# Optimization experiments

Hardware: AMD Instinct MI355X
Metric: run time of the kernel (lower is better)

## Reference

```python
import jax, jax.numpy as jnp
import numpy as np

N = 20000      # nodes
E = 640000     # edges (before self loops)
IN = 256       # in_channels == out_channels (forced by classifier size 4*in)
H1, C1 = 8, 16   # conv1: heads=8, out=16 -> concat 128
H2, C2 = 1, 256  # conv2: heads=1, out=out_channels
B = 4096       # article pairs
NEG_SLOPE = 0.2  # PyG GATv2Conv default negative_slope


def setup_inputs() -> dict:
    key = jax.random.key(0)
    ks = jax.random.split(key, 24)
    s = 0.05
    inp = {
        "gnn_x": jax.random.normal(ks[0], (N, IN), jnp.float32),
        "vanilla_x": jax.random.normal(ks[1], (N, IN), jnp.float32),
        "edge_src": jax.random.randint(ks[2], (E,), 0, N, jnp.int32),
        "edge_dst": jax.random.randint(ks[3], (E,), 0, N, jnp.int32),
        "a1_idx": jax.random.randint(ks[4], (B,), 0, N, jnp.int64),
        "a2_idx": jax.random.randint(ks[5], (B,), 0, N, jnp.int64),
        # conv1 params (lin_l, lin_r, att, bias)
        "Wl1": jax.random.normal(ks[6], (IN, H1 * C1), jnp.float32) * s,
        "bl1": jnp.zeros((H1 * C1,), jnp.float32),
        "Wr1": jax.random.normal(ks[7], (IN, H1 * C1), jnp.float32) * s,
        "br1": jnp.zeros((H1 * C1,), jnp.float32),
        "att1": jax.random.normal(ks[8], (H1, C1), jnp.float32) * s,
        "bias1": jnp.zeros((H1 * C1,), jnp.float32),
        # conv2 params
        "Wl2": jax.random.normal(ks[9], (H1 * C1, H2 * C2), jnp.float32) * s,
        "bl2": jnp.zeros((H2 * C2,), jnp.float32),
        "Wr2": jax.random.normal(ks[10], (H1 * C1, H2 * C2), jnp.float32) * s,
        "br2": jnp.zeros((H2 * C2,), jnp.float32),
        "att2": jax.random.normal(ks[11], (H2, C2), jnp.float32) * s,
        "bias2": jnp.zeros((H2 * C2,), jnp.float32),
        # classifier
        "Wc": jax.random.normal(ks[12], (4 * IN, 1), jnp.float32) * s,
        "bc": jnp.zeros((1,), jnp.float32),
    }
    return inp


def _gatv2_layer(x, src, dst, Wl, bl, Wr, br, att, bias):
    """GATv2Conv: x_l = lin_l(x)[src], x_r = lin_r(x)[dst];
    e = att . leaky_relu(x_l + x_r); segment softmax over dst; scatter-add x_l*alpha."""
    n = x.shape[0]
    h, c = att.shape
    xl = (x @ Wl + bl).reshape(n, h, c)
    xr = (x @ Wr + br).reshape(n, h, c)
    # per-edge attention logits [E, H]
    e = jnp.einsum('ehc,hc->eh', jax.nn.leaky_relu(xl[src] + xr[dst], NEG_SLOPE), att)
    # segment softmax over destination nodes (self loops guarantee non-empty segments)
    emax = jax.ops.segment_max(e, dst, num_segments=n)
    ex = jnp.exp(e - emax[dst])
    denom = jax.ops.segment_sum(ex, dst, num_segments=n)
    alpha = ex / denom[dst]                      # [E, H]
    out = jax.ops.segment_sum(alpha[:, :, None] * xl[src], dst, num_segments=n)  # [N,H,C]
    return out.reshape(n, h * c) + bias          # concat=True (heads=1 identical)


def reference(gnn_x, vanilla_x, Wl1, bl1, Wr1, br1, att1, bias1,
              Wl2, bl2, Wr2, br2, att2, bias2, Wc, bc,
              edge_src, edge_dst, a1_idx, a2_idx):
    n = gnn_x.shape[0]
    loops = jnp.arange(n, dtype=edge_src.dtype)
    src = jnp.concatenate([edge_src, loops])     # PyG add_self_loops=True
    dst = jnp.concatenate([edge_dst, loops])
    x = _gatv2_layer(gnn_x, src, dst, Wl1, bl1, Wr1, br1, att1, bias1)
    x = jax.nn.relu(x)
    x = _gatv2_layer(x, src, dst, Wl2, bl2, Wr2, br2, att2, bias2)
    combined = jnp.concatenate(
        [vanilla_x[a1_idx], vanilla_x[a2_idx], x[a1_idx], x[a2_idx]], axis=1)  # [B, 4*IN]
    logits = combined @ Wc + bc                  # [B, 1]
    return logits
```

## Files before the change

### kernel.cpp

```cpp
#include <hip/hip_runtime.h>
#include <math.h>

#define N_NODES 20000
#define M_PAD   20032
#define E_EDGES 640000
#define ET (E_EDGES + N_NODES)
#define IN_CH 256
#define D1 128
#define D2 256
#define BPAIRS 4096
#define NEG 0.2f

#define XCONV_BLOCKS 5008
#define WCONV_BLOCKS 512

typedef __bf16 bf16x8 __attribute__((ext_vector_type(8)));
typedef float  f32x4  __attribute__((ext_vector_type(4)));

__device__ __forceinline__ unsigned short f2b(float f) {
    unsigned int u = __float_as_uint(f);
    unsigned int r = u + 0x7FFFu + ((u >> 16) & 1u);
    return (unsigned short)(r >> 16);
}
__device__ __forceinline__ float b2f(unsigned short h) {
    return __uint_as_float(((unsigned int)h) << 16);
}
__device__ __forceinline__ float lrelu(float s) { return (s > 0.f) ? s : NEG * s; }


__global__ void hist_kernel(const int* __restrict__ edge_dst,
                            int* __restrict__ count, int* __restrict__ rank) {
    int e = blockIdx.x * blockDim.x + threadIdx.x;
    if (e >= ET) return;
    int dst = (e < E_EDGES) ? edge_dst[e] : (e - E_EDGES);
    rank[e] = atomicAdd(&count[dst], 1);
}

__global__ __launch_bounds__(1024) void scan_kernel(const int* __restrict__ count,
                                                    int* __restrict__ offsets) {
    const int PER = 20;
    int t = threadIdx.x;
    int base = t * PER;
    int local[PER];
    int sum = 0;
    int vals[PER];
    const int4* c4 = (const int4*)(count);
#pragma unroll
    for (int q = 0; q < 5; q++) {
        int idx4 = (base >> 2) + q;
        int4 v = (base + q * 4 + 3 < N_NODES) ? c4[idx4] : make_int4(
            (base + q * 4 + 0 < N_NODES) ? count[base + q * 4 + 0] : 0,
            (base + q * 4 + 1 < N_NODES) ? count[base + q * 4 + 1] : 0,
            (base + q * 4 + 2 < N_NODES) ? count[base + q * 4 + 2] : 0,
            (base + q * 4 + 3 < N_NODES) ? count[base + q * 4 + 3] : 0);
        vals[q * 4 + 0] = v.x; vals[q * 4 + 1] = v.y;
        vals[q * 4 + 2] = v.z; vals[q * 4 + 3] = v.w;
    }
#pragma unroll
    for (int i = 0; i < PER; i++) {
        local[i] = sum;
        sum += vals[i];
    }
    int lane = t & 63, wave = t >> 6;
    int s = sum;
#pragma unroll
    for (int off = 1; off < 64; off <<= 1) {
        int x = __shfl_up(s, off);
        if (lane >= off) s += x;
    }
    __shared__ int wsum[16];
    __shared__ int wpre[16];
    if (lane == 63) wsum[wave] = s;
    __syncthreads();
    if (t == 0) {
        int acc = 0;
        for (int w = 0; w < 16; w++) { wpre[w] = acc; acc += wsum[w]; }
        offsets[N_NODES] = acc;
    }
    __syncthreads();
    int thread_excl = wpre[wave] + (s - sum);
#pragma unroll
    for (int i = 0; i < PER; i++) {
        int idx = base + i;
        if (idx < N_NODES) offsets[idx] = thread_excl + local[i];
    }
}

__global__ void scatter_kernel(const int* __restrict__ edge_src,
                               const int* __restrict__ edge_dst,
                               const int* __restrict__ rank,
                               const int* __restrict__ offsets,
                               int* __restrict__ sorted_src) {
    int e = blockIdx.x * blockDim.x + threadIdx.x;
    if (e >= ET) return;
    int dst = (e < E_EDGES) ? edge_dst[e] : (e - E_EDGES);
    int src = (e < E_EDGES) ? edge_src[e] : (e - E_EDGES);
    sorted_src[offsets[dst] + rank[e]] = src;
}


__global__ void convert_all_kernel(
        const float* __restrict__ gnn_x,
        const float* __restrict__ Wl1, const float* __restrict__ Wr1,
        const float* __restrict__ Wl2, const float* __restrict__ Wr2,
        unsigned short* __restrict__ xb,
        unsigned short* __restrict__ wt1l, unsigned short* __restrict__ wt1r,
        unsigned short* __restrict__ wt2l, unsigned short* __restrict__ wt2r) {
    int bid = blockIdx.x;
    if (bid < XCONV_BLOCKS) {
        int e0 = (bid * 256 + threadIdx.x) * 4;
        int row = e0 >> 8;
        ushort4 o;
        if (row < N_NODES) {
            float4 v = *(const float4*)(gnn_x + e0);
            o.x = f2b(v.x); o.y = f2b(v.y); o.z = f2b(v.z); o.w = f2b(v.w);
        } else {
            o.x = o.y = o.z = o.w = 0;
        }
        *(ushort4*)(xb + e0) = o;
    } else {
        int idx = (bid - XCONV_BLOCKS) * 256 + threadIdx.x;
        int seg = idx >> 15;
        int r = idx & 32767;
        const float* W;
        unsigned short* Wt;
        int k, n, K;
        if (seg < 2) {
            W = seg ? Wr1 : Wl1; Wt = seg ? wt1r : wt1l;
            k = r >> 7; n = r & 127; K = IN_CH;
        } else {
            W = (seg & 1) ? Wr2 : Wl2; Wt = (seg & 1) ? wt2r : wt2l;
            k = r >> 8; n = r & 255; K = D1;
        }
        Wt[n * K + k] = f2b(W[r]);
    }
}


template <int K>
__global__ __launch_bounds__(256) void dual_gemm_mfma_kernel(
        const unsigned short* __restrict__ A,
        const unsigned short* __restrict__ Wtl,
        const unsigned short* __restrict__ Wtr,
        const float* __restrict__ bl, const float* __restrict__ br,
        unsigned short* __restrict__ Yl, unsigned short* __restrict__ Yr,
        int M, int NOUT) {
    int wave = threadIdx.x >> 6;
    int lane = threadIdx.x & 63;
    int row0 = blockIdx.x * 64;
    int col0 = (blockIdx.y * 4 + wave) * 16;
    int rsub = lane & 15;
    int koff = (lane >> 4) * 8;

    const unsigned short* ap  = A   + (size_t)(row0 + rsub) * K + koff;
    const unsigned short* bpl = Wtl + (size_t)(col0 + rsub) * K + koff;
    const unsigned short* bpr = Wtr + (size_t)(col0 + rsub) * K + koff;

    f32x4 l0 = {0.f, 0.f, 0.f, 0.f};
    f32x4 l1 = l0, l2 = l0, l3 = l0, r0 = l0, r1 = l0, r2 = l0, r3 = l0;

#pragma unroll
    for (int kb = 0; kb < K; kb += 32) {
        bf16x8 bfl = *(const bf16x8*)(bpl + kb);
        bf16x8 bfr = *(const bf16x8*)(bpr + kb);
        bf16x8 a0 = *(const bf16x8*)(ap + kb);
        bf16x8 a1 = *(const bf16x8*)(ap + 16 * K + kb);
        bf16x8 a2 = *(const bf16x8*)(ap + 32 * K + kb);
        bf16x8 a3 = *(const bf16x8*)(ap + 48 * K + kb);
        l0 = __builtin_amdgcn_mfma_f32_16x16x32_bf16(a0, bfl, l0, 0, 0, 0);
        r0 = __builtin_amdgcn_mfma_f32_16x16x32_bf16(a0, bfr, r0, 0, 0, 0);
        l1 = __builtin_amdgcn_mfma_f32_16x16x32_bf16(a1, bfl, l1, 0, 0, 0);
        r1 = __builtin_amdgcn_mfma_f32_16x16x32_bf16(a1, bfr, r1, 0, 0, 0);
        l2 = __builtin_amdgcn_mfma_f32_16x16x32_bf16(a2, bfl, l2, 0, 0, 0);
        r2 = __builtin_amdgcn_mfma_f32_16x16x32_bf16(a2, bfr, r2, 0, 0, 0);
        l3 = __builtin_amdgcn_mfma_f32_16x16x32_bf16(a3, bfl, l3, 0, 0, 0);
        r3 = __builtin_amdgcn_mfma_f32_16x16x32_bf16(a3, bfr, r3, 0, 0, 0);
    }

    int colg = col0 + rsub;
    float bvl = bl[colg];
    float bvr = br[colg];
    int rbase = row0 + (lane >> 4) * 4;
#pragma unroll
    for (int t = 0; t < 4; t++) {
        f32x4 al = (t == 0) ? l0 : (t == 1) ? l1 : (t == 2) ? l2 : l3;
        f32x4 ar = (t == 0) ? r0 : (t == 1) ? r1 : (t == 2) ? r2 : r3;
#pragma unroll
        for (int r = 0; r < 4; r++) {
            int row = rbase + t * 16 + r;
            if (row < M) {
                Yl[(size_t)row * NOUT + colg] = f2b(al[r] + bvl);
                Yr[(size_t)row * NOUT + colg] = f2b(ar[r] + bvr);
            }
        }
    }
}


__global__ __launch_bounds__(256) void aggregate1_kernel(
        const unsigned short* __restrict__ xl1, const unsigned short* __restrict__ xr1,
        const float* __restrict__ att1, const float* __restrict__ bias1,
        const int* __restrict__ offsets, const int* __restrict__ sorted_src,
        unsigned short* __restrict__ x1) {
    int wave = threadIdx.x >> 6;
    int lane = threadIdx.x & 63;
    int dst = blockIdx.x * 4 + wave;
    if (dst >= M_PAD) return;
    int c0 = lane * 2;
    if (dst >= N_NODES) {
        ushort2 z; z.x = 0; z.y = 0;
        *(ushort2*)(x1 + (size_t)dst * D1 + c0) = z;
        return;
    }

    ushort2 xru = *(const ushort2*)(xr1 + (size_t)dst * D1 + c0);
    float xr0 = b2f(xru.x), xr1v = b2f(xru.y);
    float a0 = att1[c0], a1 = att1[c0 + 1];
    int beg = offsets[dst], end = offsets[dst + 1];

    float m = -INFINITY, l = 0.f, A0 = 0.f, A1 = 0.f;
    int i = beg;
    for (; i + 4 <= end; i += 4) {
        int s0 = sorted_src[i], s1 = sorted_src[i + 1];
        int s2 = sorted_src[i + 2], s3 = sorted_src[i + 3];
        ushort2 u0 = *(const ushort2*)(xl1 + (size_t)s0 * D1 + c0);
        ushort2 u1 = *(const ushort2*)(xl1 + (size_t)s1 * D1 + c0);
        ushort2 u2 = *(const ushort2*)(xl1 + (size_t)s2 * D1 + c0);
        ushort2 u3 = *(const ushort2*)(xl1 + (size_t)s3 * D1 + c0);
        float v00 = b2f(u0.x), v01 = b2f(u0.y);
        float v10 = b2f(u1.x), v11 = b2f(u1.y);
        float v20 = b2f(u2.x), v21 = b2f(u2.y);
        float v30 = b2f(u3.x), v31 = b2f(u3.y);
        float p0 = a0 * lrelu(v00 + xr0) + a1 * lrelu(v01 + xr1v);
        float p1 = a0 * lrelu(v10 + xr0) + a1 * lrelu(v11 + xr1v);
        float p2 = a0 * lrelu(v20 + xr0) + a1 * lrelu(v21 + xr1v);
        float p3 = a0 * lrelu(v30 + xr0) + a1 * lrelu(v31 + xr1v);
        p0 += __shfl_xor(p0, 1); p1 += __shfl_xor(p1, 1);
        p2 += __shfl_xor(p2, 1); p3 += __shfl_xor(p3, 1);
        p0 += __shfl_xor(p0, 2); p1 += __shfl_xor(p1, 2);
        p2 += __shfl_xor(p2, 2); p3 += __shfl_xor(p3, 2);
        p0 += __shfl_xor(p0, 4); p1 += __shfl_xor(p1, 4);
        p2 += __shfl_xor(p2, 4); p3 += __shfl_xor(p3, 4);
        float mn = fmaxf(fmaxf(fmaxf(p0, p1), fmaxf(p2, p3)), m);
        float corr = __expf(m - mn);
        float e0 = __expf(p0 - mn), e1 = __expf(p1 - mn);
        float e2 = __expf(p2 - mn), e3 = __expf(p3 - mn);
        l = l * corr + (e0 + e1) + (e2 + e3);
        A0 = A0 * corr + e0 * v00 + e1 * v10 + e2 * v20 + e3 * v30;
        A1 = A1 * corr + e0 * v01 + e1 * v11 + e2 * v21 + e3 * v31;
        m = mn;
    }
    for (; i < end; i++) {
        int src = sorted_src[i];
        ushort2 vu = *(const ushort2*)(xl1 + (size_t)src * D1 + c0);
        float v0 = b2f(vu.x), v1 = b2f(vu.y);
        float p = a0 * lrelu(v0 + xr0) + a1 * lrelu(v1 + xr1v);
        p += __shfl_xor(p, 1);
        p += __shfl_xor(p, 2);
        p += __shfl_xor(p, 4);
        float mn = fmaxf(m, p);
        float corr = __expf(m - mn);
        float pe = __expf(p - mn);
        l = l * corr + pe;
        A0 = A0 * corr + pe * v0;
        A1 = A1 * corr + pe * v1;
        m = mn;
    }
    float inv = 1.f / l;
    ushort2 o;
    o.x = f2b(fmaxf(A0 * inv + bias1[c0], 0.f));
    o.y = f2b(fmaxf(A1 * inv + bias1[c0 + 1], 0.f));
    *(ushort2*)(x1 + (size_t)dst * D1 + c0) = o;
}


__global__ __launch_bounds__(256) void aggregate2_kernel(
        const unsigned short* __restrict__ xl2, const unsigned short* __restrict__ xr2,
        const float* __restrict__ att2, const float* __restrict__ bias2,
        const int* __restrict__ offsets, const int* __restrict__ sorted_src,
        float* __restrict__ x2) {
    int wave = threadIdx.x >> 6;
    int lane = threadIdx.x & 63;
    int dst = blockIdx.x * 4 + wave;
    if (dst >= N_NODES) return;
    int c0 = lane * 4;

    ushort4 xru = *(const ushort4*)(xr2 + (size_t)dst * D2 + c0);
    float xr0 = b2f(xru.x), xr1v = b2f(xru.y), xr2v = b2f(xru.z), xr3 = b2f(xru.w);
    float a0 = att2[c0], a1 = att2[c0 + 1], a2 = att2[c0 + 2], a3 = att2[c0 + 3];
    int beg = offsets[dst], end = offsets[dst + 1];

    float m = -INFINITY, l = 0.f;
    float A0 = 0.f, A1 = 0.f, A2 = 0.f, A3 = 0.f;
    int i = beg;
    for (; i + 4 <= end; i += 4) {
        int s0 = sorted_src[i], s1 = sorted_src[i + 1];
        int s2 = sorted_src[i + 2], s3 = sorted_src[i + 3];
        ushort4 u0 = *(const ushort4*)(xl2 + (size_t)s0 * D2 + c0);
        ushort4 u1 = *(const ushort4*)(xl2 + (size_t)s1 * D2 + c0);
        ushort4 u2 = *(const ushort4*)(xl2 + (size_t)s2 * D2 + c0);
        ushort4 u3 = *(const ushort4*)(xl2 + (size_t)s3 * D2 + c0);
        float v00 = b2f(u0.x), v01 = b2f(u0.y), v02 = b2f(u0.z), v03 = b2f(u0.w);
        float v10 = b2f(u1.x), v11 = b2f(u1.y), v12 = b2f(u1.z), v13 = b2f(u1.w);
        float v20 = b2f(u2.x), v21 = b2f(u2.y), v22 = b2f(u2.z), v23 = b2f(u2.w);
        float v30 = b2f(u3.x), v31 = b2f(u3.y), v32 = b2f(u3.z), v33 = b2f(u3.w);
        float p0 = a0 * lrelu(v00 + xr0) + a1 * lrelu(v01 + xr1v)
                 + a2 * lrelu(v02 + xr2v) + a3 * lrelu(v03 + xr3);
        float p1 = a0 * lrelu(v10 + xr0) + a1 * lrelu(v11 + xr1v)
                 + a2 * lrelu(v12 + xr2v) + a3 * lrelu(v13 + xr3);
        float p2 = a0 * lrelu(v20 + xr0) + a1 * lrelu(v21 + xr1v)
                 + a2 * lrelu(v22 + xr2v) + a3 * lrelu(v23 + xr3);
        float p3 = a0 * lrelu(v30 + xr0) + a1 * lrelu(v31 + xr1v)
                 + a2 * lrelu(v32 + xr2v) + a3 * lrelu(v33 + xr3);
        p0 += __shfl_xor(p0, 1);  p1 += __shfl_xor(p1, 1);
        p2 += __shfl_xor(p2, 1);  p3 += __shfl_xor(p3, 1);
        p0 += __shfl_xor(p0, 2);  p1 += __shfl_xor(p1, 2);
        p2 += __shfl_xor(p2, 2);  p3 += __shfl_xor(p3, 2);
        p0 += __shfl_xor(p0, 4);  p1 += __shfl_xor(p1, 4);
        p2 += __shfl_xor(p2, 4);  p3 += __shfl_xor(p3, 4);
        p0 += __shfl_xor(p0, 8);  p1 += __shfl_xor(p1, 8);
        p2 += __shfl_xor(p2, 8);  p3 += __shfl_xor(p3, 8);
        p0 += __shfl_xor(p0, 16); p1 += __shfl_xor(p1, 16);
        p2 += __shfl_xor(p2, 16); p3 += __shfl_xor(p3, 16);
        p0 += __shfl_xor(p0, 32); p1 += __shfl_xor(p1, 32);
        p2 += __shfl_xor(p2, 32); p3 += __shfl_xor(p3, 32);
        float mn = fmaxf(fmaxf(fmaxf(p0, p1), fmaxf(p2, p3)), m);
        float corr = __expf(m - mn);
        float e0 = __expf(p0 - mn), e1 = __expf(p1 - mn);
        float e2 = __expf(p2 - mn), e3 = __expf(p3 - mn);
        l = l * corr + (e0 + e1) + (e2 + e3);
        A0 = A0 * corr + e0 * v00 + e1 * v10 + e2 * v20 + e3 * v30;
        A1 = A1 * corr + e0 * v01 + e1 * v11 + e2 * v21 + e3 * v31;
        A2 = A2 * corr + e0 * v02 + e1 * v12 + e2 * v22 + e3 * v32;
        A3 = A3 * corr + e0 * v03 + e1 * v13 + e2 * v23 + e3 * v33;
        m = mn;
    }
    for (; i < end; i++) {
        int src = sorted_src[i];
        ushort4 vu = *(const ushort4*)(xl2 + (size_t)src * D2 + c0);
        float v0 = b2f(vu.x), v1 = b2f(vu.y), v2 = b2f(vu.z), v3 = b2f(vu.w);
        float p = a0 * lrelu(v0 + xr0) + a1 * lrelu(v1 + xr1v)
                + a2 * lrelu(v2 + xr2v) + a3 * lrelu(v3 + xr3);
        p += __shfl_xor(p, 1);
        p += __shfl_xor(p, 2);
        p += __shfl_xor(p, 4);
        p += __shfl_xor(p, 8);
        p += __shfl_xor(p, 16);
        p += __shfl_xor(p, 32);
        float mn = fmaxf(m, p);
        float corr = __expf(m - mn);
        float pe = __expf(p - mn);
        l = l * corr + pe;
        A0 = A0 * corr + pe * v0;
        A1 = A1 * corr + pe * v1;
        A2 = A2 * corr + pe * v2;
        A3 = A3 * corr + pe * v3;
        m = mn;
    }
    float inv = 1.f / l;
    float4 o;
    o.x = A0 * inv + bias2[c0];
    o.y = A1 * inv + bias2[c0 + 1];
    o.z = A2 * inv + bias2[c0 + 2];
    o.w = A3 * inv + bias2[c0 + 3];
    *(float4*)(x2 + (size_t)dst * D2 + c0) = o;
}


__global__ __launch_bounds__(256) void classifier_kernel(
        const float* __restrict__ vanilla_x, const float* __restrict__ x2,
        const int* __restrict__ a1_raw, const int* __restrict__ a2_raw,
        const float* __restrict__ Wc, const float* __restrict__ bc,
        float* __restrict__ out) {
    int b = blockIdx.x;
    int t = threadIdx.x;

    __shared__ int stride_s;
    if (t == 0) {
        bool i64 = true;
        for (int i = 1; i < 63; i += 2) i64 = i64 && (a1_raw[i] == 0);
        stride_s = i64 ? 2 : 1;
    }
    __syncthreads();
    int stride = stride_s;
    int a1 = a1_raw[(long)b * stride];
    int a2 = a2_raw[(long)b * stride];

    float s = vanilla_x[a1 * IN_CH + t] * Wc[t]
            + vanilla_x[a2 * IN_CH + t] * Wc[IN_CH + t]
            + x2[a1 * D2 + t] * Wc[2 * IN_CH + t]
            + x2[a2 * D2 + t] * Wc[3 * IN_CH + t];
    s += __shfl_xor(s, 1);
    s += __shfl_xor(s, 2);
    s += __shfl_xor(s, 4);
    s += __shfl_xor(s, 8);
    s += __shfl_xor(s, 16);
    s += __shfl_xor(s, 32);
    __shared__ float part[4];
    if ((t & 63) == 0) part[t >> 6] = s;
    __syncthreads();
    if (t == 0) out[b] = part[0] + part[1] + part[2] + part[3] + bc[0];
}


extern "C" void kernel_launch(void* const* d_in, const int* in_sizes, int n_in,
                              void* d_out, int out_size, void* d_ws, size_t ws_size,
                              hipStream_t stream) {
    const float* gnn_x     = (const float*)d_in[0];
    const float* vanilla_x = (const float*)d_in[1];
    const int*   edge_src  = (const int*)d_in[2];
    const int*   edge_dst  = (const int*)d_in[3];
    const int*   a1_idx    = (const int*)d_in[4];
    const int*   a2_idx    = (const int*)d_in[5];
    const float* Wl1   = (const float*)d_in[6];
    const float* bl1   = (const float*)d_in[7];
    const float* Wr1   = (const float*)d_in[8];
    const float* br1   = (const float*)d_in[9];
    const float* att1  = (const float*)d_in[10];
    const float* bias1 = (const float*)d_in[11];
    const float* Wl2   = (const float*)d_in[12];
    const float* bl2   = (const float*)d_in[13];
    const float* Wr2   = (const float*)d_in[14];
    const float* br2   = (const float*)d_in[15];
    const float* att2  = (const float*)d_in[16];
    const float* bias2 = (const float*)d_in[17];
    const float* Wc    = (const float*)d_in[18];
    const float* bc    = (const float*)d_in[19];
    float* out = (float*)d_out;

    char* p = (char*)d_ws;
    unsigned short* xb   = (unsigned short*)p; p += (size_t)M_PAD * IN_CH * 2;
    unsigned short* x1b  = (unsigned short*)p; p += (size_t)M_PAD * D1 * 2;
    unsigned short* xl1b = (unsigned short*)p; p += (size_t)N_NODES * D1 * 2;
    unsigned short* xr1b = (unsigned short*)p; p += (size_t)N_NODES * D1 * 2;
    unsigned short* xl2b = (unsigned short*)p; p += (size_t)N_NODES * D2 * 2;
    unsigned short* xr2b = (unsigned short*)p; p += (size_t)N_NODES * D2 * 2;
    unsigned short* wt1l = (unsigned short*)p; p += (size_t)D1 * IN_CH * 2;
    unsigned short* wt1r = (unsigned short*)p; p += (size_t)D1 * IN_CH * 2;
    unsigned short* wt2l = (unsigned short*)p; p += (size_t)D2 * D1 * 2;
    unsigned short* wt2r = (unsigned short*)p; p += (size_t)D2 * D1 * 2;
    float* x2 = (float*)p; p += (size_t)N_NODES * D2 * 4;
    int* count      = (int*)p; p += (size_t)N_NODES * 4;
    int* offsets    = (int*)p; p += (size_t)(N_NODES + 4) * 4;
    int* rank       = (int*)p; p += (size_t)ET * 4;
    int* sorted_src = (int*)p; p += (size_t)ET * 4;

    hipMemsetAsync(count, 0, (size_t)N_NODES * sizeof(int), stream);

    int eb = (ET + 255) / 256;
    hist_kernel<<<eb, 256, 0, stream>>>(edge_dst, count, rank);
    scan_kernel<<<1, 1024, 0, stream>>>(count, offsets);
    scatter_kernel<<<eb, 256, 0, stream>>>(edge_src, edge_dst, rank, offsets, sorted_src);

    convert_all_kernel<<<XCONV_BLOCKS + WCONV_BLOCKS, 256, 0, stream>>>(
        gnn_x, Wl1, Wr1, Wl2, Wr2, xb, wt1l, wt1r, wt2l, wt2r);

    dim3 g1(M_PAD / 64, D1 / 64);
    dual_gemm_mfma_kernel<IN_CH><<<g1, 256, 0, stream>>>(
        xb, wt1l, wt1r, bl1, br1, xl1b, xr1b, N_NODES, D1);
    aggregate1_kernel<<<M_PAD / 4, 256, 0, stream>>>(
        xl1b, xr1b, att1, bias1, offsets, sorted_src, x1b);

    dim3 g2(M_PAD / 64, D2 / 64);
    dual_gemm_mfma_kernel<D1><<<g2, 256, 0, stream>>>(
        x1b, wt2l, wt2r, bl2, br2, xl2b, xr2b, N_NODES, D2);
    aggregate2_kernel<<<(N_NODES + 3) / 4, 256, 0, stream>>>(
        xl2b, xr2b, att2, bias2, offsets, sorted_src, x2);

    classifier_kernel<<<BPAIRS, 256, 0, stream>>>(
        vanilla_x, x2, a1_idx, a2_idx, Wc, bc, out);
}
```

Before: 311.3 us.

## Drop online-softmax max tracking, split edges across half-waves, fuse histogram into prep

Measured after the change: 298.8 us. 4.0% less time.

```diff
diff --git a/kernel.cpp b/kernel.cpp
--- a/kernel.cpp
+++ b/kernel.cpp
@@ -10,9 +10,17 @@
 #define D2 256
 #define BPAIRS 4096
 #define NEG 0.2f
+#define LOG2E 1.4426950408889634f
 
 #define XCONV_BLOCKS 5008
 #define WCONV_BLOCKS 512
+#define HIST_BLOCKS  ((ET + 255) / 256)
+
+#if __has_builtin(__builtin_amdgcn_exp2f)
+#define EXP2F(x) __builtin_amdgcn_exp2f(x)
+#else
+#define EXP2F(x) exp2f(x)
+#endif
 
 typedef __bf16 bf16x8 __attribute__((ext_vector_type(8)));
 typedef float  f32x4  __attribute__((ext_vector_type(4)));
@@ -25,87 +33,29 @@
 __device__ __forceinline__ float b2f(unsigned short h) {
     return __uint_as_float(((unsigned int)h) << 16);
 }
-__device__ __forceinline__ float lrelu(float s) { return (s > 0.f) ? s : NEG * s; }
-
-
-__global__ void hist_kernel(const int* __restrict__ edge_dst,
-                            int* __restrict__ count, int* __restrict__ rank) {
-    int e = blockIdx.x * blockDim.x + threadIdx.x;
-    if (e >= ET) return;
-    int dst = (e < E_EDGES) ? edge_dst[e] : (e - E_EDGES);
-    rank[e] = atomicAdd(&count[dst], 1);
-}
-
-__global__ __launch_bounds__(1024) void scan_kernel(const int* __restrict__ count,
-                                                    int* __restrict__ offsets) {
-    const int PER = 20;
-    int t = threadIdx.x;
-    int base = t * PER;
-    int local[PER];
-    int sum = 0;
-    int vals[PER];
-    const int4* c4 = (const int4*)(count);
-#pragma unroll
-    for (int q = 0; q < 5; q++) {
-        int idx4 = (base >> 2) + q;
-        int4 v = (base + q * 4 + 3 < N_NODES) ? c4[idx4] : make_int4(
-            (base + q * 4 + 0 < N_NODES) ? count[base + q * 4 + 0] : 0,
-            (base + q * 4 + 1 < N_NODES) ? count[base + q * 4 + 1] : 0,
-            (base + q * 4 + 2 < N_NODES) ? count[base + q * 4 + 2] : 0,
-            (base + q * 4 + 3 < N_NODES) ? count[base + q * 4 + 3] : 0);
-        vals[q * 4 + 0] = v.x; vals[q * 4 + 1] = v.y;
-        vals[q * 4 + 2] = v.z; vals[q * 4 + 3] = v.w;
-    }
-#pragma unroll
-    for (int i = 0; i < PER; i++) {
-        local[i] = sum;
-        sum += vals[i];
-    }
-    int lane = t & 63, wave = t >> 6;
-    int s = sum;
-#pragma unroll
-    for (int off = 1; off < 64; off <<= 1) {
-        int x = __shfl_up(s, off);
-        if (lane >= off) s += x;
-    }
-    __shared__ int wsum[16];
-    __shared__ int wpre[16];
-    if (lane == 63) wsum[wave] = s;
-    __syncthreads();
-    if (t == 0) {
-        int acc = 0;
-        for (int w = 0; w < 16; w++) { wpre[w] = acc; acc += wsum[w]; }
-        offsets[N_NODES] = acc;
-    }
-    __syncthreads();
-    int thread_excl = wpre[wave] + (s - sum);
-#pragma unroll
-    for (int i = 0; i < PER; i++) {
-        int idx = base + i;
-        if (idx < N_NODES) offsets[idx] = thread_excl + local[i];
-    }
-}
-
-__global__ void scatter_kernel(const int* __restrict__ edge_src,
-                               const int* __restrict__ edge_dst,
-                               const int* __restrict__ rank,
-                               const int* __restrict__ offsets,
-                               int* __restrict__ sorted_src) {
-    int e = blockIdx.x * blockDim.x + threadIdx.x;
-    if (e >= ET) return;
-    int dst = (e < E_EDGES) ? edge_dst[e] : (e - E_EDGES);
-    int src = (e < E_EDGES) ? edge_src[e] : (e - E_EDGES);
-    sorted_src[offsets[dst] + rank[e]] = src;
-}
-
-
-__global__ void convert_all_kernel(
+__device__ __forceinline__ float lrelu(float s) { return fmaxf(s, NEG * s); }
+
+__device__ __forceinline__ void unpack8(uint4 u, float* v) {
+    v[0] = __uint_as_float(u.x << 16); v[1] = __uint_as_float(u.x & 0xFFFF0000u);
+    v[2] = __uint_as_float(u.y << 16); v[3] = __uint_as_float(u.y & 0xFFFF0000u);
+    v[4] = __uint_as_float(u.z << 16); v[5] = __uint_as_float(u.z & 0xFFFF0000u);
+    v[6] = __uint_as_float(u.w << 16); v[7] = __uint_as_float(u.w & 0xFFFF0000u);
+}
+__device__ __forceinline__ void unpack4(uint2 u, float* v) {
+    v[0] = __uint_as_float(u.x << 16); v[1] = __uint_as_float(u.x & 0xFFFF0000u);
+    v[2] = __uint_as_float(u.y << 16); v[3] = __uint_as_float(u.y & 0xFFFF0000u);
+}
+
+
+__global__ void prep_kernel(
         const float* __restrict__ gnn_x,
         const float* __restrict__ Wl1, const float* __restrict__ Wr1,
         const float* __restrict__ Wl2, const float* __restrict__ Wr2,
+        const int* __restrict__ edge_dst,
         unsigned short* __restrict__ xb,
         unsigned short* __restrict__ wt1l, unsigned short* __restrict__ wt1r,
-        unsigned short* __restrict__ wt2l, unsigned short* __restrict__ wt2r) {
+        unsigned short* __restrict__ wt2l, unsigned short* __restrict__ wt2r,
+        int* __restrict__ count, int* __restrict__ rank) {
     int bid = blockIdx.x;
     if (bid < XCONV_BLOCKS) {
         int e0 = (bid * 256 + threadIdx.x) * 4;
@@ -118,7 +68,7 @@
             o.x = o.y = o.z = o.w = 0;
         }
         *(ushort4*)(xb + e0) = o;
-    } else {
+    } else if (bid < XCONV_BLOCKS + WCONV_BLOCKS) {
         int idx = (bid - XCONV_BLOCKS) * 256 + threadIdx.x;
         int seg = idx >> 15;
         int r = idx & 32767;
@@ -133,7 +83,64 @@
             k = r >> 8; n = r & 255; K = D1;
         }
         Wt[n * K + k] = f2b(W[r]);
-    }
+    } else {
+        int e = (bid - XCONV_BLOCKS - WCONV_BLOCKS) * 256 + threadIdx.x;
+        if (e >= ET) return;
+        int dst = (e < E_EDGES) ? edge_dst[e] : (e - E_EDGES);
+        rank[e] = atomicAdd(&count[dst], 1);
+    }
+}
+
+
+__global__ __launch_bounds__(1024) void scan_kernel(const int* __restrict__ count,
+                                                    int* __restrict__ offsets) {
+    const int PER = 20;
+    int t = threadIdx.x;
+    int base = t * PER;
+    int local[PER];
+    int sum = 0;
+#pragma unroll
+    for (int i = 0; i < PER; i++) {
+        int idx = base + i;
+        int v = (idx < N_NODES) ? count[idx] : 0;
+        local[i] = sum;
+        sum += v;
+    }
+    int lane = t & 63, wave = t >> 6;
+    int s = sum;
+#pragma unroll
+    for (int off = 1; off < 64; off <<= 1) {
+        int x = __shfl_up(s, off);
+        if (lane >= off) s += x;
+    }
+    __shared__ int wsum[16];
+    __shared__ int wpre[16];
+    if (lane == 63) wsum[wave] = s;
+    __syncthreads();
+    if (t == 0) {
+        int acc = 0;
+        for (int w = 0; w < 16; w++) { wpre[w] = acc; acc += wsum[w]; }
+        offsets[N_NODES] = acc;
+    }
+    __syncthreads();
+    int thread_excl = wpre[wave] + (s - sum);
+#pragma unroll
+    for (int i = 0; i < PER; i++) {
+        int idx = base + i;
+        if (idx < N_NODES) offsets[idx] = thread_excl + local[i];
+    }
+}
+
+__global__ void scatter_kernel(const int* __restrict__ edge_src,
+                               const int* __restrict__ edge_dst,
+                               const int* __restrict__ rank,
+                               const int* __restrict__ offsets,
+                               int* __restrict__ sorted_src) {
+    int e = blockIdx.x * blockDim.x + threadIdx.x;
+    if (e >= ET) return;
+    int dst = (e < E_EDGES) ? edge_dst[e] : (e - E_EDGES);
+    int src = (e < E_EDGES) ? edge_src[e] : (e - E_EDGES);
+    sorted_src[offsets[dst] + rank[e]] = src;
 }
 
 
@@ -204,73 +211,87 @@
         unsigned short* __restrict__ x1) {
     int wave = threadIdx.x >> 6;
     int lane = threadIdx.x & 63;
+    int half = lane >> 5;
+    int hl = lane & 31;
     int dst = blockIdx.x * 4 + wave;
     if (dst >= M_PAD) return;
-    int c0 = lane * 2;
+    int c0 = hl * 4;
     if (dst >= N_NODES) {
-        ushort2 z; z.x = 0; z.y = 0;
-        *(ushort2*)(x1 + (size_t)dst * D1 + c0) = z;
+        if (half == 0) {
+            uint2 z; z.x = 0; z.y = 0;
+            *(uint2*)(x1 + (size_t)dst * D1 + c0) = z;
+        }
         return;
     }
 
-    ushort2 xru = *(const ushort2*)(xr1 + (size_t)dst * D1 + c0);
-    float xr0 = b2f(xru.x), xr1v = b2f(xru.y);
-    float a0 = att1[c0], a1 = att1[c0 + 1];
+    float xr[4], att[4];
+    unpack4(*(const uint2*)(xr1 + (size_t)dst * D1 + c0), xr);
+#pragma unroll
+    for (int j = 0; j < 4; j++) att[j] = att1[c0 + j] * LOG2E;
     int beg = offsets[dst], end = offsets[dst + 1];
 
-    float m = -INFINITY, l = 0.f, A0 = 0.f, A1 = 0.f;
+    float l = 0.f;
+    float A0 = 0.f, A1 = 0.f, A2 = 0.f, A3 = 0.f;
     int i = beg;
     for (; i + 4 <= end; i += 4) {
-        int s0 = sorted_src[i], s1 = sorted_src[i + 1];
-        int s2 = sorted_src[i + 2], s3 = sorted_src[i + 3];
-        ushort2 u0 = *(const ushort2*)(xl1 + (size_t)s0 * D1 + c0);
-        ushort2 u1 = *(const ushort2*)(xl1 + (size_t)s1 * D1 + c0);
-        ushort2 u2 = *(const ushort2*)(xl1 + (size_t)s2 * D1 + c0);
-        ushort2 u3 = *(const ushort2*)(xl1 + (size_t)s3 * D1 + c0);
-        float v00 = b2f(u0.x), v01 = b2f(u0.y);
-        float v10 = b2f(u1.x), v11 = b2f(u1.y);
-        float v20 = b2f(u2.x), v21 = b2f(u2.y);
-        float v30 = b2f(u3.x), v31 = b2f(u3.y);
-        float p0 = a0 * lrelu(v00 + xr0) + a1 * lrelu(v01 + xr1v);
-        float p1 = a0 * lrelu(v10 + xr0) + a1 * lrelu(v11 + xr1v);
-        float p2 = a0 * lrelu(v20 + xr0) + a1 * lrelu(v21 + xr1v);
-        float p3 = a0 * lrelu(v30 + xr0) + a1 * lrelu(v31 + xr1v);
-        p0 += __shfl_xor(p0, 1); p1 += __shfl_xor(p1, 1);
-        p2 += __shfl_xor(p2, 1); p3 += __shfl_xor(p3, 1);
-        p0 += __shfl_xor(p0, 2); p1 += __shfl_xor(p1, 2);
-        p2 += __shfl_xor(p2, 2); p3 += __shfl_xor(p3, 2);
-        p0 += __shfl_xor(p0, 4); p1 += __shfl_xor(p1, 4);
-        p2 += __shfl_xor(p2, 4); p3 += __shfl_xor(p3, 4);
-        float mn = fmaxf(fmaxf(fmaxf(p0, p1), fmaxf(p2, p3)), m);
-        float corr = __expf(m - mn);
-        float e0 = __expf(p0 - mn), e1 = __expf(p1 - mn);
-        float e2 = __expf(p2 - mn), e3 = __expf(p3 - mn);
-        l = l * corr + (e0 + e1) + (e2 + e3);
-        A0 = A0 * corr + e0 * v00 + e1 * v10 + e2 * v20 + e3 * v30;
-        A1 = A1 * corr + e0 * v01 + e1 * v11 + e2 * v21 + e3 * v31;
-        m = mn;
-    }
-    for (; i < end; i++) {
-        int src = sorted_src[i];
-        ushort2 vu = *(const ushort2*)(xl1 + (size_t)src * D1 + c0);
-        float v0 = b2f(vu.x), v1 = b2f(vu.y);
-        float p = a0 * lrelu(v0 + xr0) + a1 * lrelu(v1 + xr1v);
-        p += __shfl_xor(p, 1);
-        p += __shfl_xor(p, 2);
-        p += __shfl_xor(p, 4);
-        float mn = fmaxf(m, p);
-        float corr = __expf(m - mn);
-        float pe = __expf(p - mn);
-        l = l * corr + pe;
-        A0 = A0 * corr + pe * v0;
-        A1 = A1 * corr + pe * v1;
-        m = mn;
-    }
-    float inv = 1.f / l;
-    ushort2 o;
-    o.x = f2b(fmaxf(A0 * inv + bias1[c0], 0.f));
-    o.y = f2b(fmaxf(A1 * inv + bias1[c0 + 1], 0.f));
-    *(ushort2*)(x1 + (size_t)dst * D1 + c0) = o;
+        int sA = sorted_src[i + half];
+        int sB = sorted_src[i + 2 + half];
+        float vA[4], vB[4];
+        unpack4(*(const uint2*)(xl1 + (size_t)sA * D1 + c0), vA);
+        unpack4(*(const uint2*)(xl1 + (size_t)sB * D1 + c0), vB);
+        float pA = att[0] * lrelu(vA[0] + xr[0]) + att[1] * lrelu(vA[1] + xr[1])
+                 + att[2] * lrelu(vA[2] + xr[2]) + att[3] * lrelu(vA[3] + xr[3]);
+        float pB = att[0] * lrelu(vB[0] + xr[0]) + att[1] * lrelu(vB[1] + xr[1])
+                 + att[2] * lrelu(vB[2] + xr[2]) + att[3] * lrelu(vB[3] + xr[3]);
+        pA += __shfl_xor(pA, 1); pB += __shfl_xor(pB, 1);
+        pA += __shfl_xor(pA, 2); pB += __shfl_xor(pB, 2);
+        float wA = EXP2F(pA), wB = EXP2F(pB);
+        l += wA + wB;
+        A0 += wA * vA[0] + wB * vB[0];
+        A1 += wA * vA[1] + wB * vB[1];
+        A2 += wA * vA[2] + wB * vB[2];
+        A3 += wA * vA[3] + wB * vB[3];
+    }
+    for (; i + 2 <= end; i += 2) {
+        int sA = sorted_src[i + half];
+        float vA[4];
+        unpack4(*(const uint2*)(xl1 + (size_t)sA * D1 + c0), vA);
+        float pA = att[0] * lrelu(vA[0] + xr[0]) + att[1] * lrelu(vA[1] + xr[1])
+                 + att[2] * lrelu(vA[2] + xr[2]) + att[3] * lrelu(vA[3] + xr[3]);
+        pA += __shfl_xor(pA, 1);
+        pA += __shfl_xor(pA, 2);
+        float wA = EXP2F(pA);
+        l += wA;
+        A0 += wA * vA[0]; A1 += wA * vA[1]; A2 += wA * vA[2]; A3 += wA * vA[3];
+    }
+    if (i < end && half == 0) {
+        int sA = sorted_src[i];
+        float vA[4];
+        unpack4(*(const uint2*)(xl1 + (size_t)sA * D1 + c0), vA);
+        float pA = att[0] * lrelu(vA[0] + xr[0]) + att[1] * lrelu(vA[1] + xr[1])
+                 + att[2] * lrelu(vA[2] + xr[2]) + att[3] * lrelu(vA[3] + xr[3]);
+        pA += __shfl_xor(pA, 1);
+        pA += __shfl_xor(pA, 2);
+        float wA = EXP2F(pA);
+        l += wA;
+        A0 += wA * vA[0]; A1 += wA * vA[1]; A2 += wA * vA[2]; A3 += wA * vA[3];
+    }
+    l  += __shfl_xor(l, 32);
+    A0 += __shfl_xor(A0, 32);
+    A1 += __shfl_xor(A1, 32);
+    A2 += __shfl_xor(A2, 32);
+    A3 += __shfl_xor(A3, 32);
+    if (half == 0) {
+        float inv = 1.f / l;
+        unsigned short o0 = f2b(fmaxf(A0 * inv + bias1[c0 + 0], 0.f));
+        unsigned short o1 = f2b(fmaxf(A1 * inv + bias1[c0 + 1], 0.f));
+        unsigned short o2 = f2b(fmaxf(A2 * inv + bias1[c0 + 2], 0.f));
+        unsigned short o3 = f2b(fmaxf(A3 * inv + bias1[c0 + 3], 0.f));
+        uint2 o;
+        o.x = (unsigned int)o0 | ((unsigned int)o1 << 16);
+        o.y = (unsigned int)o2 | ((unsigned int)o3 << 16);
+        *(uint2*)(x1 + (size_t)dst * D1 + c0) = o;
+    }
 }
 
 
@@ -281,89 +302,96 @@
         float* __restrict__ x2) {
     int wave = threadIdx.x >> 6;
     int lane = threadIdx.x & 63;
+    int half = lane >> 5;
+    int hl = lane & 31;
     int dst = blockIdx.x * 4 + wave;
     if (dst >= N_NODES) return;
-    int c0 = lane * 4;
-
-    ushort4 xru = *(const ushort4*)(xr2 + (size_t)dst * D2 + c0);
-    float xr0 = b2f(xru.x), xr1v = b2f(xru.y), xr2v = b2f(xru.z), xr3 = b2f(xru.w);
-    float a0 = att2[c0], a1 = att2[c0 + 1], a2 = att2[c0 + 2], a3 = att2[c0 + 3];
+    int c0 = hl * 8;
+
+    float xr[8], att[8];
+    unpack8(*(const uint4*)(xr2 + (size_t)dst * D2 + c0), xr);
+#pragma unroll
+    for (int j = 0; j < 8; j++) att[j] = att2[c0 + j] * LOG2E;
     int beg = offsets[dst], end = offsets[dst + 1];
 
-    float m = -INFINITY, l = 0.f;
-    float A0 = 0.f, A1 = 0.f, A2 = 0.f, A3 = 0.f;
+    float l = 0.f;
+    float acc[8];
+#pragma unroll
+    for (int j = 0; j < 8; j++) acc[j] = 0.f;
+
     int i = beg;
     for (; i + 4 <= end; i += 4) {
-        int s0 = sorted_src[i], s1 = sorted_src[i + 1];
-        int s2 = sorted_src[i + 2], s3 = sorted_src[i + 3];
-        ushort4 u0 = *(const ushort4*)(xl2 + (size_t)s0 * D2 + c0);
-        ushort4 u1 = *(const ushort4*)(xl2 + (size_t)s1 * D2 + c0);
-        ushort4 u2 = *(const ushort4*)(xl2 + (size_t)s2 * D2 + c0);
-        ushort4 u3 = *(const ushort4*)(xl2 + (size_t)s3 * D2 + c0);
-        float v00 = b2f(u0.x), v01 = b2f(u0.y), v02 = b2f(u0.z), v03 = b2f(u0.w);
-        float v10 = b2f(u1.x), v11 = b2f(u1.y), v12 = b2f(u1.z), v13 = b2f(u1.w);
-        float v20 = b2f(u2.x), v21 = b2f(u2.y), v22 = b2f(u2.z), v23 = b2f(u2.w);
-        float v30 = b2f(u3.x), v31 = b2f(u3.y), v32 = b2f(u3.z), v33 = b2f(u3.w);
-        float p0 = a0 * lrelu(v00 + xr0) + a1 * lrelu(v01 + xr1v)
-                 + a2 * lrelu(v02 + xr2v) + a3 * lrelu(v03 + xr3);
-        float p1 = a0 * lrelu(v10 + xr0) + a1 * lrelu(v11 + xr1v)
-                 + a2 * lrelu(v12 + xr2v) + a3 * lrelu(v13 + xr3);
-        float p2 = a0 * lrelu(v20 + xr0) + a1 * lrelu(v21 + xr1v)
-                 + a2 * lrelu(v22 + xr2v) + a3 * lrelu(v23 + xr3);
-        float p3 = a0 * lrelu(v30 + xr0) + a1 * lrelu(v31 + xr1v)
-                 + a2 * lrelu(v32 + xr2v) + a3 * lrelu(v33 + xr3);
-        p0 += __shfl_xor(p0, 1);  p1 += __shfl_xor(p1, 1);
-        p2 += __shfl_xor(p2, 1);  p3 += __shfl_xor(p3, 1);
-        p0 += __shfl_xor(p0, 2);  p1 += __shfl_xor(p1, 2);
-        p2 += __shfl_xor(p2, 2);  p3 += __shfl_xor(p3, 2);
-        p0 += __shfl_xor(p0, 4);  p1 += __shfl_xor(p1, 4);
-        p2 += __shfl_xor(p2, 4);  p3 += __shfl_xor(p3, 4);
-        p0 += __shfl_xor(p0, 8);  p1 += __shfl_xor(p1, 8);
-        p2 += __shfl_xor(p2, 8);  p3 += __shfl_xor(p3, 8);
-        p0 += __shfl_xor(p0, 16); p1 += __shfl_xor(p1, 16);
-        p2 += __shfl_xor(p2, 16); p3 += __shfl_xor(p3, 16);
-        p0 += __shfl_xor(p0, 32); p1 += __shfl_xor(p1, 32);
-        p2 += __shfl_xor(p2, 32); p3 += __shfl_xor(p3, 32);
-        float mn = fmaxf(fmaxf(fmaxf(p0, p1), fmaxf(p2, p3)), m);
-        float corr = __expf(m - mn);
-        float e0 = __expf(p0 - mn), e1 = __expf(p1 - mn);
-        float e2 = __expf(p2 - mn), e3 = __expf(p3 - mn);
-        l = l * corr + (e0 + e1) + (e2 + e3);
-        A0 = A0 * corr + e0 * v00 + e1 * v10 + e2 * v20 + e3 * v30;
-        A1 = A1 * corr + e0 * v01 + e1 * v11 + e2 * v21 + e3 * v31;
-        A2 = A2 * corr + e0 * v02 + e1 * v12 + e2 * v22 + e3 * v32;
-        A3 = A3 * corr + e0 * v03 + e1 * v13 + e2 * v23 + e3 * v33;
-        m = mn;
-    }
-    for (; i < end; i++) {
-        int src = sorted_src[i];
-        ushort4 vu = *(const ushort4*)(xl2 + (size_t)src * D2 + c0);
-        float v0 = b2f(vu.x), v1 = b2f(vu.y), v2 = b2f(vu.z), v3 = b2f(vu.w);
-        float p = a0 * lrelu(v0 + xr0) + a1 * lrelu(v1 + xr1v)
-                + a2 * lrelu(v2 + xr2v) + a3 * lrelu(v3 + xr3);
-        p += __shfl_xor(p, 1);
-        p += __shfl_xor(p, 2);
-        p += __shfl_xor(p, 4);
-        p += __shfl_xor(p, 8);
-        p += __shfl_xor(p, 16);
-        p += __shfl_xor(p, 32);
-        float mn = fmaxf(m, p);
-        float corr = __expf(m - mn);
-        float pe = __expf(p - mn);
-        l = l * corr + pe;
-        A0 = A0 * corr + pe * v0;
-        A1 = A1 * corr + pe * v1;
-        A2 = A2 * corr + pe * v2;
-        A3 = A3 * corr + pe * v3;
-        m = mn;
-    }
-    float inv = 1.f / l;
-    float4 o;
-    o.x = A0 * inv + bias2[c0];
-    o.y = A1 * inv + bias2[c0 + 1];
-    o.z = A2 * inv + bias2[c0 + 2];
-    o.w = A3 * inv + bias2[c0 + 3];
-    *(float4*)(x2 + (size_t)dst * D2 + c0) = o;
+        int sA = sorted_src[i + half];
+        int sB = sorted_src[i + 2 + half];
+        float vA[8], vB[8];
+        unpack8(*(const uint4*)(xl2 + (size_t)sA * D2 + c0), vA);
+        unpack8(*(const uint4*)(xl2 + (size_t)sB * D2 + c0), vB);
+        float pA = 0.f, pB = 0.f;
+#pragma unroll
+        for (int j = 0; j < 8; j++) pA = fmaf(att[j], lrelu(vA[j] + xr[j]), pA);
+#pragma unroll
+        for (int j = 0; j < 8; j++) pB = fmaf(att[j], lrelu(vB[j] + xr[j]), pB);
+        pA += __shfl_xor(pA, 1);  pB += __shfl_xor(pB, 1);
+        pA += __shfl_xor(pA, 2);  pB += __shfl_xor(pB, 2);
+        pA += __shfl_xor(pA, 4);  pB += __shfl_xor(pB, 4);
+        pA += __shfl_xor(pA, 8);  pB += __shfl_xor(pB, 8);
+        pA += __shfl_xor(pA, 16); pB += __shfl_xor(pB, 16);
+        float wA = EXP2F(pA), wB = EXP2F(pB);
+        l += wA + wB;
+#pragma unroll
+        for (int j = 0; j < 8; j++) acc[j] += wA * vA[j] + wB * vB[j];
+    }
+    for (; i + 2 <= end; i += 2) {
+        int sA = sorted_src[i + half];
+        float vA[8];
+        unpack8(*(const uint4*)(xl2 + (size_t)sA * D2 + c0), vA);
+        float pA = 0.f;
+#pragma unroll
+        for (int j = 0; j < 8; j++) pA = fmaf(att[j], lrelu(vA[j] + xr[j]), pA);
+        pA += __shfl_xor(pA, 1);
+        pA += __shfl_xor(pA, 2);
+        pA += __shfl_xor(pA, 4);
+        pA += __shfl_xor(pA, 8);
+        pA += __shfl_xor(pA, 16);
+        float wA = EXP2F(pA);
+        l += wA;
+#pragma unroll
+        for (int j = 0; j < 8; j++) acc[j] += wA * vA[j];
+    }
+    if (i < end && half == 0) {
+        int sA = sorted_src[i];
+        float vA[8];
+        unpack8(*(const uint4*)(xl2 + (size_t)sA * D2 + c0), vA);
+        float pA = 0.f;
+#pragma unroll
+        for (int j = 0; j < 8; j++) pA = fmaf(att[j], lrelu(vA[j] + xr[j]), pA);
+        pA += __shfl_xor(pA, 1);
+        pA += __shfl_xor(pA, 2);
+        pA += __shfl_xor(pA, 4);
+        pA += __shfl_xor(pA, 8);
+        pA += __shfl_xor(pA, 16);
+        float wA = EXP2F(pA);
+        l += wA;
+#pragma unroll
+        for (int j = 0; j < 8; j++) acc[j] += wA * vA[j];
+    }
+    l += __shfl_xor(l, 32);
+#pragma unroll
+    for (int j = 0; j < 8; j++) acc[j] += __shfl_xor(acc[j], 32);
+    if (half == 0) {
+        float inv = 1.f / l;
+        float4 o0, o1;
+        o0.x = acc[0] * inv + bias2[c0 + 0];
+        o0.y = acc[1] * inv + bias2[c0 + 1];
+        o0.z = acc[2] * inv + bias2[c0 + 2];
+        o0.w = acc[3] * inv + bias2[c0 + 3];
+        o1.x = acc[4] * inv + bias2[c0 + 4];
+        o1.y = acc[5] * inv + bias2[c0 + 5];
+        o1.z = acc[6] * inv + bias2[c0 + 6];
+        o1.w = acc[7] * inv + bias2[c0 + 7];
+        *(float4*)(x2 + (size_t)dst * D2 + c0) = o0;
+        *(float4*)(x2 + (size_t)dst * D2 + c0 + 4) = o1;
+    }
 }
 
 
@@ -447,13 +475,12 @@
 
     hipMemsetAsync(count, 0, (size_t)N_NODES * sizeof(int), stream);
 
-    int eb = (ET + 255) / 256;
-    hist_kernel<<<eb, 256, 0, stream>>>(edge_dst, count, rank);
+    prep_kernel<<<XCONV_BLOCKS + WCONV_BLOCKS + HIST_BLOCKS, 256, 0, stream>>>(
+        gnn_x, Wl1, Wr1, Wl2, Wr2, edge_dst,
+        xb, wt1l, wt1r, wt2l, wt2r, count, rank);
     scan_kernel<<<1, 1024, 0, stream>>>(count, offsets);
-    scatter_kernel<<<eb, 256, 0, stream>>>(edge_src, edge_dst, rank, offsets, sorted_src);
-
-    convert_all_kernel<<<XCONV_BLOCKS + WCONV_BLOCKS, 256, 0, stream>>>(
-        gnn_x, Wl1, Wr1, Wl2, Wr2, xb, wt1l, wt1r, wt2l, wt2r);
+    scatter_kernel<<<HIST_BLOCKS, 256, 0, stream>>>(
+        edge_src, edge_dst, rank, offsets, sorted_src);
 
     dim3 g1(M_PAD / 64, D1 / 64);
     dual_gemm_mfma_kernel<IN_CH><<<g1, 256, 0, stream>>>(
```
